# Performance work log

Hardware: AMD Instinct MI355X
Metric: run time of the kernel (lower is better)

The kernel has to match this reference:

```python
import jax, jax.numpy as jnp
import numpy as np

LMBDA = 100.0
GAMMA = 0.5


def _get_mask(evals1, evals2, gamma):
    # evals1, evals2: [B, K]; returns D: [B, K, K]
    scale = jnp.maximum(jnp.max(evals1, axis=1), jnp.max(evals2, axis=1))[:, None]
    e1 = evals1 / scale
    e2 = evals2 / scale
    g1 = (e1 ** gamma)[:, None, :]   # [B, 1, K]
    g2 = (e2 ** gamma)[:, :, None]   # [B, K, 1]
    M_re = g2 / (g2 ** 2 + 1) - g1 / (g1 ** 2 + 1)
    M_im = 1.0 / (g2 ** 2 + 1) - 1.0 / (g1 ** 2 + 1)
    return M_re ** 2 + M_im ** 2


def setup_inputs() -> dict:
    key = jax.random.key(0)
    ks = jax.random.split(key, 6)
    B, Vx, Vy, C, K = 8, 20000, 20000, 256, 128
    return {
        "feat_x": jax.random.normal(ks[0], (B, Vx, C), dtype=jnp.float32),
        "feat_y": jax.random.normal(ks[1], (B, Vy, C), dtype=jnp.float32),
        "evals_x": jax.random.uniform(ks[2], (B, K), dtype=jnp.float32, minval=0.01, maxval=1.0),
        "evals_y": jax.random.uniform(ks[3], (B, K), dtype=jnp.float32, minval=0.01, maxval=1.0),
        "evecs_trans_x": jax.random.normal(ks[4], (B, K, Vx), dtype=jnp.float32),
        "evecs_trans_y": jax.random.normal(ks[5], (B, K, Vy), dtype=jnp.float32),
    }


def reference(feat_x, feat_y, evals_x, evals_y, evecs_trans_x, evecs_trans_y):
    # Spectral projections of features
    A = jnp.einsum('bkv,bvc->bkc', evecs_trans_x, feat_x)   # [B, K, C]
    Bm = jnp.einsum('bkv,bvc->bkc', evecs_trans_y, feat_y)  # [B, K, C]
    D = _get_mask(evals_x, evals_y, GAMMA)                  # [B, K, K]
    AAt = jnp.einsum('bkc,bjc->bkj', A, A)                  # [B, K, K]
    BAt = jnp.einsum('bkc,bjc->bkj', Bm, A)                 # [B, K, K]
    # Batched over (B, i): solve (AAt + lmbda*diag(D[b,i])) x = BAt[b,i]
    Dmats = jax.vmap(jax.vmap(jnp.diag))(D)                 # [B, K, K, K]
    M = AAt[:, None, :, :] + LMBDA * Dmats                  # [B, K, K, K]
    Cxy = jnp.linalg.solve(M, BAt[..., None])[..., 0]       # rows: Cxy[b, i, :]
    return Cxy
```

## Files before the change

kernel.cpp:

```cpp
#include <hip/hip_runtime.h>
#include <hip/hip_bf16.h>

namespace {

constexpr int NB = 8;
constexpr int NV = 20000;
constexpr int NC = 256;
constexpr int NK = 128;
constexpr float LMBDA = 100.0f;
constexpr int KSTEP = 32;
constexpr int CHUNKS = 16;

typedef __attribute__((ext_vector_type(8))) short bf16x8;
typedef __attribute__((ext_vector_type(4))) float f32x4;

__device__ __forceinline__ uint cvtpk(float a, float c) {
  uint r;
  asm("v_cvt_pk_bf16_f32 %0, %1, %2" : "=v"(r) : "v"(a), "v"(c));
  return r;
}

template <int MODE>
__global__ __launch_bounds__(256, 2) void proj_mfma(
    const float* __restrict__ Ex, const float* __restrict__ Fx,
    const float* __restrict__ Ey, const float* __restrict__ Fy,
    float* __restrict__ A, float* __restrict__ Bm, float* __restrict__ P)
{
  extern __shared__ ushort smem[];

  const int chunk = blockIdx.x;
  const int ct    = blockIdx.y;
  const int bs    = blockIdx.z;
  const int b     = bs >> 1;
  const int side  = bs & 1;
  const float* __restrict__ E = (side ? Ey : Ex) + (size_t)b * NK * NV;
  const float* __restrict__ F = (side ? Fy : Fx) + (size_t)b * NV * NC;
  float* __restrict__ Out = (side ? Bm : A) + (size_t)b * NK * NC;
  const int cb = ct * 128;

  const int start = chunk * 39 + (chunk > 0 ? 1 : 0);
  const int nsteps = 39 + (chunk == 0 ? 1 : 0);
  const int v0 = start * KSTEP;

  const int tid  = threadIdx.x;
  const int lane = tid & 63;
  const int w    = tid >> 6;
  const int wm   = w >> 1;
  const int wn   = w & 1;
  const int lrow = lane >> 4;
  const int lcol = lane & 15;

  const int erow = tid >> 1;
  const int eh   = tid & 1;
  const float* Erow = E + (size_t)erow * NV + v0 + eh * 16;

  const int bg  = tid >> 6;
  const int c0  = (tid & 63) * 2;
  const int c1  = c0 + 1;
  const float* Fbase = F + (size_t)(v0 + bg * 8) * NC + cb + c0;

  f32x4 acc[4][4];
#pragma unroll
  for (int fi = 0; fi < 4; fi++)
#pragma unroll
    for (int ni = 0; ni < 4; ni++) acc[fi][ni] = (f32x4)0.f;

  const int entA = (((lcol) + lrow * 4) & 15) + lrow * 16;

  auto loadE = [&](int t, float4* e) {
    const float* p = Erow + t * KSTEP;
    e[0] = *(const float4*)(p);
    e[1] = *(const float4*)(p + 4);
    e[2] = *(const float4*)(p + 8);
    e[3] = *(const float4*)(p + 12);
  };
  auto loadF = [&](int t, float2* f) {
    const float* p = Fbase + (size_t)t * KSTEP * NC;
#pragma unroll
    for (int j = 0; j < 8; j++) f[j] = *(const float2*)(p + (size_t)j * NC);
  };

  auto stage = [&](int buf, const float4* e, const float2* f) {
    ushort* AHb = smem + buf * 16384;
    ushort* BHb = AHb + 8192;
    {
      const int frag = erow >> 4;
      const int r15  = erow & 15;
#pragma unroll
      for (int i = 0; i < 2; i++) {
        const int vg  = 2 * eh + i;
        const int ent = ((r15 + vg * 4) & 15) + vg * 16;
        const float4 x = e[2 * i];
        const float4 y = e[2 * i + 1];
        uint h0 = cvtpk(x.x, x.y), h1 = cvtpk(x.z, x.w);
        uint h2 = cvtpk(y.x, y.y), h3 = cvtpk(y.z, y.w);
        uint l0 = cvtpk(x.x - __uint_as_float(h0 << 16),
                        x.y - __uint_as_float(h0 & 0xffff0000u));
        uint l1 = cvtpk(x.z - __uint_as_float(h1 << 16),
                        x.w - __uint_as_float(h1 & 0xffff0000u));
        uint l2 = cvtpk(y.x - __uint_as_float(h2 << 16),
                        y.y - __uint_as_float(h2 & 0xffff0000u));
        uint l3 = cvtpk(y.z - __uint_as_float(h3 << 16),
                        y.w - __uint_as_float(h3 & 0xffff0000u));
        *(uint4*)(AHb + frag * 512 + ent * 8)        = make_uint4(h0, h1, h2, h3);
        *(uint4*)(AHb + 4096 + frag * 512 + ent * 8) = make_uint4(l0, l1, l2, l3);
      }
    }
    {
      const int frag = c0 >> 4;
      const int ent0 = (((c0 & 15) + frag) & 15) + bg * 16;
      const int ent1 = (((c1 & 15) + frag) & 15) + bg * 16;
      uint h0[4], l0[4], h1[4], l1[4];
#pragma unroll
      for (int i = 0; i < 4; i++) {
        const float a0 = f[2 * i].x, b0 = f[2 * i + 1].x;
        const float a1 = f[2 * i].y, b1 = f[2 * i + 1].y;
        uint h = cvtpk(a0, b0);
        h0[i] = h;
        l0[i] = cvtpk(a0 - __uint_as_float(h << 16),
                      b0 - __uint_as_float(h & 0xffff0000u));
        h = cvtpk(a1, b1);
        h1[i] = h;
        l1[i] = cvtpk(a1 - __uint_as_float(h << 16),
                      b1 - __uint_as_float(h & 0xffff0000u));
      }
      *(uint4*)(BHb + frag * 512 + ent0 * 8)        = make_uint4(h0[0], h0[1], h0[2], h0[3]);
      *(uint4*)(BHb + 4096 + frag * 512 + ent0 * 8) = make_uint4(l0[0], l0[1], l0[2], l0[3]);
      *(uint4*)(BHb + frag * 512 + ent1 * 8)        = make_uint4(h1[0], h1[1], h1[2], h1[3]);
      *(uint4*)(BHb + 4096 + frag * 512 + ent1 * 8) = make_uint4(l1[0], l1[1], l1[2], l1[3]);
    }
  };

  auto domfma = [&](int buf) {
    const ushort* AHb = smem + buf * 16384;
    const ushort* BHb = AHb + 8192;
    bf16x8 bHf[4], bLf[4];
#pragma unroll
    for (int ni = 0; ni < 4; ni++) {
      int cg = wn * 4 + ni;
      int entB = ((lcol + cg) & 15) + lrow * 16;
      bHf[ni] = *(const bf16x8*)(BHb + cg * 512 + entB * 8);
      bLf[ni] = *(const bf16x8*)(BHb + 4096 + cg * 512 + entB * 8);
    }
#pragma unroll
    for (int fi = 0; fi < 4; fi++) {
      bf16x8 aH = *(const bf16x8*)(AHb + (wm * 4 + fi) * 512 + entA * 8);
      bf16x8 aL = *(const bf16x8*)(AHb + 4096 + (wm * 4 + fi) * 512 + entA * 8);
#pragma unroll
      for (int ni = 0; ni < 4; ni++) {
        acc[fi][ni] = __builtin_amdgcn_mfma_f32_16x16x32_bf16(aH, bHf[ni], acc[fi][ni], 0, 0, 0);
        acc[fi][ni] = __builtin_amdgcn_mfma_f32_16x16x32_bf16(aH, bLf[ni], acc[fi][ni], 0, 0, 0);
        acc[fi][ni] = __builtin_amdgcn_mfma_f32_16x16x32_bf16(aL, bHf[ni], acc[fi][ni], 0, 0, 0);
      }
    }
  };

  float4 eA[4]; float2 fA[8];
  float4 eB[4]; float2 fB[8];
  loadE(0, eA); loadF(0, fA);
  stage(0, eA, fA);
  {
    const int t1 = (1 < nsteps) ? 1 : 0;
    loadE(t1, eB); loadF(t1, fB);
  }
  __syncthreads();

  for (int s = 0; s < nsteps; s++) {
    const int bufc = s & 1;
    if (s + 1 < nsteps) {
      if ((s & 1) == 0) stage(bufc ^ 1, eB, fB);
      else              stage(bufc ^ 1, eA, fA);
    }
    if (s + 2 < nsteps) {
      if ((s & 1) == 0) { loadE(s + 2, eA); loadF(s + 2, fA); }
      else              { loadE(s + 2, eB); loadF(s + 2, fB); }
    }
    domfma(bufc);
    __syncthreads();
  }

#pragma unroll
  for (int fi = 0; fi < 4; fi++) {
#pragma unroll
    for (int ni = 0; ni < 4; ni++) {
      const float* av = (const float*)&acc[fi][ni];
#pragma unroll
      for (int q = 0; q < 4; q++) {
        int row = wm * 64 + fi * 16 + lrow * 4 + q;
        int col = cb + wn * 64 + ni * 16 + lcol;
        if (MODE == 0) {
          P[(((size_t)chunk * 16 + bs) * NK + row) * NC + col] = av[q];
        } else {
          atomicAdd(&Out[(size_t)row * NC + col], av[q]);
        }
      }
    }
  }
}

__global__ __launch_bounds__(256) void reduce_kernel(
    const float* __restrict__ P, float* __restrict__ AB)
{
  const int g = blockIdx.x * 256 + threadIdx.x;
  const int bsi = g >> 13;
  const int rem4 = g & 8191;
  const int side = bsi & 1, b = bsi >> 1;
  float4 s = make_float4(0.f, 0.f, 0.f, 0.f);
#pragma unroll
  for (int ch = 0; ch < CHUNKS; ch++) {
    float4 v = *(const float4*)(P + (((size_t)ch * 16 + bsi) * 8192 + rem4) * 4);
    s.x += v.x; s.y += v.y; s.z += v.z; s.w += v.w;
  }
  *(float4*)(AB + ((size_t)side * 262144 + (size_t)b * 8192 * 4 + (size_t)rem4 * 4)) = s;
}

__global__ __launch_bounds__(256) void gram_kernel(
    const float* __restrict__ A, const float* __restrict__ Bm,
    float* __restrict__ AAt, float* __restrict__ BAt)
{
  const int i0 = blockIdx.x * 8;
  const int b  = blockIdx.y;
  __shared__ float Xi[16][260];
  const float* __restrict__ Ab = A  + (size_t)b * NK * NC;
  const float* __restrict__ Bb = Bm + (size_t)b * NK * NC;
  const int tid = threadIdx.x;
  for (int idx = tid; idx < 16 * 64; idx += 256) {
    int row = idx >> 6, c4 = idx & 63;
    const float* src = (row < 8) ? (Ab + (size_t)(i0 + row) * NC)
                                 : (Bb + (size_t)(i0 + row - 8) * NC);
    *(float4*)&Xi[row][c4 * 4] = *(const float4*)(src + c4 * 4);
  }
  __syncthreads();
  const int j = tid & 127;
  const int m = tid >> 7;
  const float* __restrict__ Arow = Ab + (size_t)j * NC;
  float accv[8];
#pragma unroll
  for (int i = 0; i < 8; i++) accv[i] = 0.f;
  for (int c4 = 0; c4 < 64; c4++) {
    float4 a4 = *(const float4*)(Arow + c4 * 4);
#pragma unroll
    for (int i = 0; i < 8; i++) {
      float4 x4 = *(const float4*)&Xi[m * 8 + i][c4 * 4];
      accv[i] = fmaf(x4.x, a4.x, accv[i]);
      accv[i] = fmaf(x4.y, a4.y, accv[i]);
      accv[i] = fmaf(x4.z, a4.z, accv[i]);
      accv[i] = fmaf(x4.w, a4.w, accv[i]);
    }
  }
  float* Outp = (m ? BAt : AAt) + ((size_t)b * NK + i0) * NK + j;
#pragma unroll
  for (int i = 0; i < 8; i++) Outp[(size_t)i * NK] = accv[i];
}

__global__ __launch_bounds__(256) void mask_kernel(
    const float* __restrict__ evx, const float* __restrict__ evy,
    float* __restrict__ Dm)
{
  const int b = blockIdx.x;
  const int tid = threadIdx.x;
  __shared__ float red[256];
  __shared__ float t1x[128], t2x[128], t1y[128], t2y[128];
  float v = (tid < 128) ? evx[b * 128 + tid] : evy[b * 128 + (tid - 128)];
  red[tid] = v;
  __syncthreads();
  for (int sft = 128; sft > 0; sft >>= 1) {
    if (tid < sft) red[tid] = fmaxf(red[tid], red[tid + sft]);
    __syncthreads();
  }
  const float inv_scale = 1.0f / red[0];
  if (tid < 128) {
    float e = evx[b * 128 + tid] * inv_scale;
    float g = sqrtf(e);
    float d = 1.f / (g * g + 1.f);
    t1x[tid] = g * d;  t2x[tid] = d;
  } else {
    int i = tid - 128;
    float e = evy[b * 128 + i] * inv_scale;
    float g = sqrtf(e);
    float d = 1.f / (g * g + 1.f);
    t1y[i] = g * d;  t2y[i] = d;
  }
  __syncthreads();
  float* __restrict__ Db = Dm + (size_t)b * NK * NK;
  for (int idx = tid; idx < NK * NK; idx += 256) {
    int i = idx >> 7, jj = idx & 127;
    float re = t1y[i] - t1x[jj];
    float im = t2y[i] - t2x[jj];
    Db[idx] = re * re + im * im;
  }
}

__global__ __launch_bounds__(512) void invert_kernel(
    const float* __restrict__ AAt, float* __restrict__ Sinv)
{
  extern __shared__ float sh[];
  float* M = sh;
  float* R = sh + 128 * 132;
  const int b = blockIdx.x;
  const int tid = threadIdx.x;
  const float* __restrict__ Sb = AAt + (size_t)b * NK * NK;
  for (int idx = tid; idx < NK * NK; idx += 512) {
    M[(idx >> 7) * 132 + (idx & 127)] = Sb[idx];
  }
  __syncthreads();
  const int r = tid & 127;
  const int h = tid >> 7;
  const int c0 = h * 32;

  for (int p = 0; p < 16; p++) {
    const int J0 = p * 8;
    const bool inJ = (r >= J0) && (r < J0 + 8);
    const int i0 = r - J0;

    float g[8][8];
#pragma unroll
    for (int i = 0; i < 8; i++)
#pragma unroll
      for (int j = 0; j < 8; j++) g[i][j] = M[(J0 + i) * 132 + J0 + j];

#pragma unroll
    for (int j = 0; j < 8; j++) {
      const float invd = 1.f / g[j][j];
#pragma unroll
      for (int i = 0; i < 8; i++) {
        if (i == j) continue;
        const float f = g[i][j] * invd;
#pragma unroll
        for (int c = 0; c < 8; c++) {
          if (c == j) continue;
          g[i][c] = fmaf(-f, g[j][c], g[i][c]);
        }
        g[i][j] = -f;
      }
#pragma unroll
      for (int c = 0; c < 8; c++) {
        if (c == j) continue;
        g[j][c] *= invd;
      }
      g[j][j] = invd;
    }

    float c8[8];
    if (inJ) {
#pragma unroll
      for (int q = 0; q < 8; q++) {
        float v = 0.f;
#pragma unroll
        for (int i = 0; i < 8; i++)
          if (i0 == i) v = g[i][q];
        c8[q] = ((i0 == q) ? 1.f : 0.f) - v;
      }
    } else {
      float mr8[8];
#pragma unroll
      for (int k = 0; k < 8; k++) mr8[k] = M[r * 132 + J0 + k];
#pragma unroll
      for (int q = 0; q < 8; q++) {
        float a = 0.f;
#pragma unroll
        for (int k = 0; k < 8; k++) a = fmaf(mr8[k], g[k][q], a);
        c8[q] = a;
      }
    }

    if (inJ) {
#pragma unroll
      for (int i = 0; i < 8; i++)
        *(float4*)&R[i0 * 132 + c0 + i * 4] = *(const float4*)&M[r * 132 + c0 + i * 4];
    }
    __syncthreads();

    float4 m[8];
#pragma unroll
    for (int i = 0; i < 8; i++) m[i] = *(const float4*)&M[r * 132 + c0 + i * 4];
#pragma unroll
    for (int k = 0; k < 8; k++) {
      const float f = c8[k];
#pragma unroll
      for (int i = 0; i < 8; i++) {
        float4 rv = *(const float4*)&R[k * 132 + c0 + i * 4];
        m[i].x = fmaf(-f, rv.x, m[i].x);
        m[i].y = fmaf(-f, rv.y, m[i].y);
        m[i].z = fmaf(-f, rv.z, m[i].z);
        m[i].w = fmaf(-f, rv.w, m[i].w);
      }
    }
    {
      const bool panelH = (h == (J0 >> 5));
      const int q4 = (J0 & 31) >> 2;
      float sp[8];
#pragma unroll
      for (int q = 0; q < 8; q++)
        sp[q] = -c8[q] + ((inJ && i0 == q) ? 1.f : 0.f);
      const float4 lo = make_float4(sp[0], sp[1], sp[2], sp[3]);
      const float4 hi = make_float4(sp[4], sp[5], sp[6], sp[7]);
#pragma unroll
      for (int i = 0; i < 8; i++) {
        if (panelH && i == q4)     m[i] = lo;
        if (panelH && i == q4 + 1) m[i] = hi;
      }
    }
#pragma unroll
    for (int i = 0; i < 8; i++) *(float4*)&M[r * 132 + c0 + i * 4] = m[i];
    __syncthreads();
  }

  float* __restrict__ Ob = Sinv + (size_t)b * NK * NK;
  for (int idx = tid; idx < NK * NK; idx += 512) {
    Ob[idx] = M[(idx >> 7) * 132 + (idx & 127)];
  }
}

__global__ __launch_bounds__(256) void ns_kernel(
    const float* __restrict__ AAt, const float* __restrict__ Xin,
    float* __restrict__ Xout)
{
  extern __shared__ float sh[];
  float* S_ = sh;
  float* X_ = sh + 128 * 132;
  float* W_ = X_ + 128 * 133;
  const int tile = blockIdx.x;
  const int b    = blockIdx.y;
  const int j0   = tile * 32;
  const int tid  = threadIdx.x;
  const float* __restrict__ Sg = AAt + (size_t)b * NK * NK;
  const float* __restrict__ Xg = Xin + (size_t)b * NK * NK;
  float* __restrict__ Og       = Xout + (size_t)b * NK * NK;
  for (int idx = tid; idx < NK * NK; idx += 256) {
    int rr = idx >> 7, cc = idx & 127;
    S_[rr * 132 + cc] = Sg[idx];
    X_[rr * 133 + cc] = Xg[idx];
  }
  __syncthreads();

  const int kg  = tid >> 4;
  const int jj2 = (tid & 15) * 2;

  float aw[8][2];
#pragma unroll
  for (int u = 0; u < 8; u++) { aw[u][0] = 0.f; aw[u][1] = 0.f; }
  for (int m = 0; m < NK; m++) {
    const float x0 = X_[m * 133 + j0 + jj2];
    const float x1 = X_[m * 133 + j0 + jj2 + 1];
    float4 s0 = *(const float4*)&S_[m * 132 + kg * 8];
    float4 s1 = *(const float4*)&S_[m * 132 + kg * 8 + 4];
    const float sv[8] = {s0.x, s0.y, s0.z, s0.w, s1.x, s1.y, s1.z, s1.w};
#pragma unroll
    for (int u = 0; u < 8; u++) {
      aw[u][0] = fmaf(sv[u], x0, aw[u][0]);
      aw[u][1] = fmaf(sv[u], x1, aw[u][1]);
    }
  }
#pragma unroll
  for (int u = 0; u < 8; u++) {
#pragma unroll
    for (int j = 0; j < 2; j++) {
      const int k = kg * 8 + u;
      float val = -aw[u][j];
      if (k == j0 + jj2 + j) val += 2.f;
      W_[k * 33 + jj2 + j] = val;
    }
  }
  __syncthreads();

  float ax[8][2];
#pragma unroll
  for (int u = 0; u < 8; u++) { ax[u][0] = 0.f; ax[u][1] = 0.f; }
  for (int k = 0; k < NK; k++) {
    const float w0 = W_[k * 33 + jj2];
    const float w1 = W_[k * 33 + jj2 + 1];
#pragma unroll
    for (int u = 0; u < 8; u++) {
      const float x = X_[(kg * 8 + u) * 133 + k];
      ax[u][0] = fmaf(x, w0, ax[u][0]);
      ax[u][1] = fmaf(x, w1, ax[u][1]);
    }
  }
#pragma unroll
  for (int u = 0; u < 8; u++) {
    Og[(size_t)(kg * 8 + u) * NK + j0 + jj2]     = ax[u][0];
    Og[(size_t)(kg * 8 + u) * NK + j0 + jj2 + 1] = ax[u][1];
  }
}

__global__ __launch_bounds__(256) void solve_kernel(
    const float* __restrict__ Sinv, const float* __restrict__ BAt,
    const float* __restrict__ Dm, float* __restrict__ Cxy)
{
  extern __shared__ float sh[];
  float* SinvS = sh;
  float* ZS    = sh + 128 * 132;
  const int tile = blockIdx.x;
  const int b    = blockIdx.y;
  const int i0b  = tile * 32;
  const int tid  = threadIdx.x;
  const float* __restrict__ Sb = Sinv + (size_t)b * NK * NK;
  const float* __restrict__ Rb = BAt  + (size_t)b * NK * NK;
  const float* __restrict__ Db = Dm   + (size_t)b * NK * NK;
  for (int idx = tid; idx < NK * NK; idx += 256) {
    SinvS[(idx >> 7) * 132 + (idx & 127)] = Sb[idx];
  }
  for (int idx = tid; idx < 32 * NK; idx += 256) {
    int rr = idx >> 7, cc = idx & 127;
    ZS[rr * 133 + cc] = Rb[(size_t)(i0b + rr) * NK + cc];
  }
  __syncthreads();

  const int il = (tid >> 4) * 2;
  const int r0 = (tid & 15) * 8;
  float Y[2][8], X[2][8];
#pragma unroll
  for (int u = 0; u < 2; u++)
#pragma unroll
    for (int v = 0; v < 8; v++) Y[u][v] = 0.f;

  for (int c = 0; c < NK; c++) {
    float4 s0 = *(const float4*)&SinvS[c * 132 + r0];
    float4 s1 = *(const float4*)&SinvS[c * 132 + r0 + 4];
#pragma unroll
    for (int u = 0; u < 2; u++) {
      float z = ZS[(il + u) * 133 + c];
      Y[u][0] = fmaf(z, s0.x, Y[u][0]);
      Y[u][1] = fmaf(z, s0.y, Y[u][1]);
      Y[u][2] = fmaf(z, s0.z, Y[u][2]);
      Y[u][3] = fmaf(z, s0.w, Y[u][3]);
      Y[u][4] = fmaf(z, s1.x, Y[u][4]);
      Y[u][5] = fmaf(z, s1.y, Y[u][5]);
      Y[u][6] = fmaf(z, s1.z, Y[u][6]);
      Y[u][7] = fmaf(z, s1.w, Y[u][7]);
    }
  }
#pragma unroll
  for (int u = 0; u < 2; u++)
#pragma unroll
    for (int v = 0; v < 8; v++) X[u][v] = Y[u][v];

  for (int it = 0; it < 2; it++) {
    __syncthreads();
#pragma unroll
    for (int u = 0; u < 2; u++) {
      const float* drow = Db + (size_t)(i0b + il + u) * NK + r0;
      float* zrow = ZS + (il + u) * 133 + r0;
#pragma unroll
      for (int v = 0; v < 8; v++) zrow[v] = LMBDA * drow[v] * X[u][v];
    }
    __syncthreads();
#pragma unroll
    for (int u = 0; u < 2; u++)
#pragma unroll
      for (int v = 0; v < 8; v++) X[u][v] = Y[u][v];
    for (int c = 0; c < NK; c++) {
      float4 s0 = *(const float4*)&SinvS[c * 132 + r0];
      float4 s1 = *(const float4*)&SinvS[c * 132 + r0 + 4];
#pragma unroll
      for (int u = 0; u < 2; u++) {
        float z = ZS[(il + u) * 133 + c];
        X[u][0] = fmaf(-z, s0.x, X[u][0]);
        X[u][1] = fmaf(-z, s0.y, X[u][1]);
        X[u][2] = fmaf(-z, s0.z, X[u][2]);
        X[u][3] = fmaf(-z, s0.w, X[u][3]);
        X[u][4] = fmaf(-z, s1.x, X[u][4]);
        X[u][5] = fmaf(-z, s1.y, X[u][5]);
        X[u][6] = fmaf(-z, s1.z, X[u][6]);
        X[u][7] = fmaf(-z, s1.w, X[u][7]);
      }
    }
  }
  float* __restrict__ Ob = Cxy + ((size_t)b * NK + i0b + il) * NK + r0;
#pragma unroll
  for (int u = 0; u < 2; u++) {
    float4 o0 = make_float4(X[u][0], X[u][1], X[u][2], X[u][3]);
    float4 o1 = make_float4(X[u][4], X[u][5], X[u][6], X[u][7]);
    *(float4*)(Ob + (size_t)u * NK)     = o0;
    *(float4*)(Ob + (size_t)u * NK + 4) = o1;
  }
}

}

extern "C" void kernel_launch(void* const* d_in, const int* in_sizes, int n_in,
                              void* d_out, int out_size, void* d_ws, size_t ws_size,
                              hipStream_t stream) {
  (void)in_sizes; (void)n_in; (void)out_size;
  const float* feat_x  = (const float*)d_in[0];
  const float* feat_y  = (const float*)d_in[1];
  const float* evals_x = (const float*)d_in[2];
  const float* evals_y = (const float*)d_in[3];
  const float* etx     = (const float*)d_in[4];
  const float* ety     = (const float*)d_in[5];
  float* out = (float*)d_out;
  float* ws  = (float*)d_ws;

  float* A    = ws;
  float* Bm   = ws + 262144;
  float* AAt  = ws + 524288;
  float* BAt  = ws + 655360;
  float* Dm   = ws + 786432;
  float* Sinv = ws + 917504;
  float* P    = ws + 1048576;
  float* Sinv2 = Bm;

  const bool use_partial = ws_size >= (size_t)(1048576 + 8388608) * 4;

  constexpr int PROJ_LDS  = 2 * 16384 * 2;
  constexpr int INV_LDS   = (128 * 132 + 8 * 132) * 4;
  constexpr int NS_LDS    = (128 * 132 + 128 * 133 + 128 * 33) * 4;
  constexpr int SOLVE_LDS = (128 * 132 + 32 * 133) * 4;
  hipFuncSetAttribute((const void*)proj_mfma<0>,
                      hipFuncAttributeMaxDynamicSharedMemorySize, PROJ_LDS);
  hipFuncSetAttribute((const void*)proj_mfma<1>,
                      hipFuncAttributeMaxDynamicSharedMemorySize, PROJ_LDS);
  hipFuncSetAttribute((const void*)invert_kernel,
                      hipFuncAttributeMaxDynamicSharedMemorySize, INV_LDS);
  hipFuncSetAttribute((const void*)ns_kernel,
                      hipFuncAttributeMaxDynamicSharedMemorySize, NS_LDS);
  hipFuncSetAttribute((const void*)solve_kernel,
                      hipFuncAttributeMaxDynamicSharedMemorySize, SOLVE_LDS);

  if (use_partial) {
    proj_mfma<0><<<dim3(CHUNKS, 2, 16), 256, PROJ_LDS, stream>>>(etx, feat_x, ety, feat_y, A, Bm, P);
    reduce_kernel<<<dim3(512), 256, 0, stream>>>(P, ws);
  } else {
    hipMemsetAsync(A, 0, (size_t)524288 * sizeof(float), stream);
    proj_mfma<1><<<dim3(CHUNKS, 2, 16), 256, PROJ_LDS, stream>>>(etx, feat_x, ety, feat_y, A, Bm, P);
  }
  gram_kernel<<<dim3(16, 8), 256, 0, stream>>>(A, Bm, AAt, BAt);
  mask_kernel<<<dim3(8), 256, 0, stream>>>(evals_x, evals_y, Dm);
  invert_kernel<<<dim3(8), 512, INV_LDS, stream>>>(AAt, Sinv);
  ns_kernel<<<dim3(4, 8), 256, NS_LDS, stream>>>(AAt, Sinv, Sinv2);
  ns_kernel<<<dim3(4, 8), 256, NS_LDS, stream>>>(AAt, Sinv2, Sinv);
  solve_kernel<<<dim3(4, 8), 256, SOLVE_LDS, stream>>>(Sinv, BAt, Dm, out);
}
```

Baseline: 272.3 us.

## Load E operand directly into MFMA registers, bypassing LDS staging

Result: slower. 505.7 us (+85.7%).

```diff
diff --git a/kernel.cpp b/kernel.cpp
--- a/kernel.cpp
+++ b/kernel.cpp
@@ -50,9 +50,7 @@
   const int lrow = lane >> 4;
   const int lcol = lane & 15;
 
-  const int erow = tid >> 1;
-  const int eh   = tid & 1;
-  const float* Erow = E + (size_t)erow * NV + v0 + eh * 16;
+  const float* Abase = E + (size_t)(wm * 64 + lcol) * NV + v0 + lrow * 8;
 
   const int bg  = tid >> 6;
   const int c0  = (tid & 63) * 2;
@@ -65,75 +63,60 @@
 #pragma unroll
     for (int ni = 0; ni < 4; ni++) acc[fi][ni] = (f32x4)0.f;
 
-  const int entA = (((lcol) + lrow * 4) & 15) + lrow * 16;
-
-  auto loadE = [&](int t, float4* e) {
-    const float* p = Erow + t * KSTEP;
-    e[0] = *(const float4*)(p);
-    e[1] = *(const float4*)(p + 4);
-    e[2] = *(const float4*)(p + 8);
-    e[3] = *(const float4*)(p + 12);
-  };
   auto loadF = [&](int t, float2* f) {
     const float* p = Fbase + (size_t)t * KSTEP * NC;
 #pragma unroll
     for (int j = 0; j < 8; j++) f[j] = *(const float2*)(p + (size_t)j * NC);
   };
 
-  auto stage = [&](int buf, const float4* e, const float2* f) {
-    ushort* AHb = smem + buf * 16384;
-    ushort* BHb = AHb + 8192;
-    {
-      const int frag = erow >> 4;
-      const int r15  = erow & 15;
-#pragma unroll
-      for (int i = 0; i < 2; i++) {
-        const int vg  = 2 * eh + i;
-        const int ent = ((r15 + vg * 4) & 15) + vg * 16;
-        const float4 x = e[2 * i];
-        const float4 y = e[2 * i + 1];
-        uint h0 = cvtpk(x.x, x.y), h1 = cvtpk(x.z, x.w);
-        uint h2 = cvtpk(y.x, y.y), h3 = cvtpk(y.z, y.w);
-        uint l0 = cvtpk(x.x - __uint_as_float(h0 << 16),
-                        x.y - __uint_as_float(h0 & 0xffff0000u));
-        uint l1 = cvtpk(x.z - __uint_as_float(h1 << 16),
-                        x.w - __uint_as_float(h1 & 0xffff0000u));
-        uint l2 = cvtpk(y.x - __uint_as_float(h2 << 16),
-                        y.y - __uint_as_float(h2 & 0xffff0000u));
-        uint l3 = cvtpk(y.z - __uint_as_float(h3 << 16),
-                        y.w - __uint_as_float(h3 & 0xffff0000u));
-        *(uint4*)(AHb + frag * 512 + ent * 8)        = make_uint4(h0, h1, h2, h3);
-        *(uint4*)(AHb + 4096 + frag * 512 + ent * 8) = make_uint4(l0, l1, l2, l3);
-      }
-    }
-    {
-      const int frag = c0 >> 4;
-      const int ent0 = (((c0 & 15) + frag) & 15) + bg * 16;
-      const int ent1 = (((c1 & 15) + frag) & 15) + bg * 16;
-      uint h0[4], l0[4], h1[4], l1[4];
-#pragma unroll
-      for (int i = 0; i < 4; i++) {
-        const float a0 = f[2 * i].x, b0 = f[2 * i + 1].x;
-        const float a1 = f[2 * i].y, b1 = f[2 * i + 1].y;
-        uint h = cvtpk(a0, b0);
-        h0[i] = h;
-        l0[i] = cvtpk(a0 - __uint_as_float(h << 16),
-                      b0 - __uint_as_float(h & 0xffff0000u));
-        h = cvtpk(a1, b1);
-        h1[i] = h;
-        l1[i] = cvtpk(a1 - __uint_as_float(h << 16),
-                      b1 - __uint_as_float(h & 0xffff0000u));
-      }
-      *(uint4*)(BHb + frag * 512 + ent0 * 8)        = make_uint4(h0[0], h0[1], h0[2], h0[3]);
-      *(uint4*)(BHb + 4096 + frag * 512 + ent0 * 8) = make_uint4(l0[0], l0[1], l0[2], l0[3]);
-      *(uint4*)(BHb + frag * 512 + ent1 * 8)        = make_uint4(h1[0], h1[1], h1[2], h1[3]);
-      *(uint4*)(BHb + 4096 + frag * 512 + ent1 * 8) = make_uint4(l1[0], l1[1], l1[2], l1[3]);
+  auto loadcvtA = [&](int t, uint4 (&ah)[4], uint4 (&al)[4]) {
+#pragma unroll
+    for (int fi = 0; fi < 4; fi++) {
+      const float* p = Abase + (size_t)fi * 16 * NV + (size_t)t * KSTEP;
+      const float4 a0 = *(const float4*)(p);
+      const float4 a1 = *(const float4*)(p + 4);
+      const uint h0 = cvtpk(a0.x, a0.y), h1 = cvtpk(a0.z, a0.w);
+      const uint h2 = cvtpk(a1.x, a1.y), h3 = cvtpk(a1.z, a1.w);
+      const uint l0 = cvtpk(a0.x - __uint_as_float(h0 << 16),
+                            a0.y - __uint_as_float(h0 & 0xffff0000u));
+      const uint l1 = cvtpk(a0.z - __uint_as_float(h1 << 16),
+                            a0.w - __uint_as_float(h1 & 0xffff0000u));
+      const uint l2 = cvtpk(a1.x - __uint_as_float(h2 << 16),
+                            a1.y - __uint_as_float(h2 & 0xffff0000u));
+      const uint l3 = cvtpk(a1.z - __uint_as_float(h3 << 16),
+                            a1.w - __uint_as_float(h3 & 0xffff0000u));
+      ah[fi] = make_uint4(h0, h1, h2, h3);
+      al[fi] = make_uint4(l0, l1, l2, l3);
     }
   };
 
-  auto domfma = [&](int buf) {
-    const ushort* AHb = smem + buf * 16384;
-    const ushort* BHb = AHb + 8192;
+  auto stageB = [&](int buf, const float2* f) {
+    ushort* BHb = smem + buf * 8192;
+    const int frag = c0 >> 4;
+    const int ent0 = (((c0 & 15) + frag) & 15) + bg * 16;
+    const int ent1 = (((c1 & 15) + frag) & 15) + bg * 16;
+    uint h0[4], l0[4], h1[4], l1[4];
+#pragma unroll
+    for (int i = 0; i < 4; i++) {
+      const float a0 = f[2 * i].x, b0 = f[2 * i + 1].x;
+      const float a1 = f[2 * i].y, b1 = f[2 * i + 1].y;
+      uint h = cvtpk(a0, b0);
+      h0[i] = h;
+      l0[i] = cvtpk(a0 - __uint_as_float(h << 16),
+                    b0 - __uint_as_float(h & 0xffff0000u));
+      h = cvtpk(a1, b1);
+      h1[i] = h;
+      l1[i] = cvtpk(a1 - __uint_as_float(h << 16),
+                    b1 - __uint_as_float(h & 0xffff0000u));
+    }
+    *(uint4*)(BHb + frag * 512 + ent0 * 8)        = make_uint4(h0[0], h0[1], h0[2], h0[3]);
+    *(uint4*)(BHb + 4096 + frag * 512 + ent0 * 8) = make_uint4(l0[0], l0[1], l0[2], l0[3]);
+    *(uint4*)(BHb + frag * 512 + ent1 * 8)        = make_uint4(h1[0], h1[1], h1[2], h1[3]);
+    *(uint4*)(BHb + 4096 + frag * 512 + ent1 * 8) = make_uint4(l1[0], l1[1], l1[2], l1[3]);
+  };
+
+  auto domfma = [&](int buf, const uint4 (&ah)[4], const uint4 (&al)[4]) {
+    const ushort* BHb = smem + buf * 8192;
     bf16x8 bHf[4], bLf[4];
 #pragma unroll
     for (int ni = 0; ni < 4; ni++) {
@@ -144,8 +127,8 @@
     }
 #pragma unroll
     for (int fi = 0; fi < 4; fi++) {
-      bf16x8 aH = *(const bf16x8*)(AHb + (wm * 4 + fi) * 512 + entA * 8);
-      bf16x8 aL = *(const bf16x8*)(AHb + 4096 + (wm * 4 + fi) * 512 + entA * 8);
+      bf16x8 aH = *(const bf16x8*)&ah[fi];
+      bf16x8 aL = *(const bf16x8*)&al[fi];
 #pragma unroll
       for (int ni = 0; ni < 4; ni++) {
         acc[fi][ni] = __builtin_amdgcn_mfma_f32_16x16x32_bf16(aH, bHf[ni], acc[fi][ni], 0, 0, 0);
@@ -155,27 +138,31 @@
     }
   };
 
-  float4 eA[4]; float2 fA[8];
-  float4 eB[4]; float2 fB[8];
-  loadE(0, eA); loadF(0, fA);
-  stage(0, eA, fA);
+  uint4 ahA[4], alA[4], ahB[4], alB[4];
+  float2 fA[8], fB[8];
+  loadF(0, fA);
+  loadcvtA(0, ahA, alA);
+  stageB(0, fA);
   {
     const int t1 = (1 < nsteps) ? 1 : 0;
-    loadE(t1, eB); loadF(t1, fB);
+    loadF(t1, fB);
+    loadcvtA(t1, ahB, alB);
   }
   __syncthreads();
 
   for (int s = 0; s < nsteps; s++) {
     const int bufc = s & 1;
-    if (s + 1 < nsteps) {
-      if ((s & 1) == 0) stage(bufc ^ 1, eB, fB);
-      else              stage(bufc ^ 1, eA, fA);
-    }
-    if (s + 2 < nsteps) {
-      if ((s & 1) == 0) { loadE(s + 2, eA); loadF(s + 2, fA); }
-      else              { loadE(s + 2, eB); loadF(s + 2, fB); }
-    }
-    domfma(bufc);
+    if ((s & 1) == 0) {
+      if (s + 1 < nsteps) stageB(bufc ^ 1, fB);
+      if (s + 2 < nsteps) loadF(s + 2, fA);
+      domfma(bufc, ahA, alA);
+      if (s + 2 < nsteps) loadcvtA(s + 2, ahA, alA);
+    } else {
+      if (s + 1 < nsteps) stageB(bufc ^ 1, fA);
+      if (s + 2 < nsteps) loadF(s + 2, fB);
+      domfma(bufc, ahB, alB);
+      if (s + 2 < nsteps) loadcvtA(s + 2, ahB, alB);
+    }
     __syncthreads();
   }
 
@@ -603,7 +590,7 @@
 
   const bool use_partial = ws_size >= (size_t)(1048576 + 8388608) * 4;
 
-  constexpr int PROJ_LDS  = 2 * 16384 * 2;
+  constexpr int PROJ_LDS  = 2 * 8192 * 2;
   constexpr int INV_LDS   = (128 * 132 + 8 * 132) * 4;
   constexpr int NS_LDS    = (128 * 132 + 128 * 133 + 128 * 33) * 4;
   constexpr int SOLVE_LDS = (128 * 132 + 32 * 133) * 4;
```
